# Performance work log

Measured on AMD Instinct MI355X. Metric: run time of the kernel, lower is better.

Reference implementation:

```python
import jax, jax.numpy as jnp
import numpy as np
from jax import lax

B, T_IN, T_OUT, E, U, V = 32, 128, 128, 512, 512, 9000


def reverse_seq(x, lens):
    # tf.reverse_sequence along time axis 1
    T = x.shape[1]
    t = jnp.arange(T)[None, :]
    idx = jnp.where(t < lens[:, None], lens[:, None] - 1 - t, t)
    return jnp.take_along_axis(x, idx[:, :, None], axis=1)


def run_lstm(x, lens, kernel, bias):
    """TF LSTMCell (gate order i,j,f,o, forget_bias=1.0) with dynamic_rnn
    length semantics: zero outputs and frozen state past seq_len."""
    T = x.shape[1]
    units = bias.shape[0] // 4
    xT = jnp.swapaxes(x, 0, 1)  # [T,B,D]
    c0 = jnp.zeros((x.shape[0], units), x.dtype)
    h0 = jnp.zeros_like(c0)

    def step(carry, xs):
        c, h = carry
        xt, t = xs
        z = jnp.concatenate([xt, h], axis=-1) @ kernel + bias
        i, j, f, o = jnp.split(z, 4, axis=-1)
        c_new = jax.nn.sigmoid(f + 1.0) * c + jax.nn.sigmoid(i) * jnp.tanh(j)
        h_new = jax.nn.sigmoid(o) * jnp.tanh(c_new)
        valid = (t < lens)[:, None]
        c2 = jnp.where(valid, c_new, c)
        h2 = jnp.where(valid, h_new, h)
        out = jnp.where(valid, h_new, 0.0)
        return (c2, h2), out

    (c, h), outs = lax.scan(step, (c0, h0), (xT, jnp.arange(T)))
    return jnp.swapaxes(outs, 0, 1), (c, h)


def setup_inputs() -> dict:
    key = jax.random.key(0)
    ks = jax.random.split(key, 20)
    s = 0.05
    inp = {
        "embed_in": jax.random.normal(ks[0], (B, T_IN, E), jnp.float32),
        "dec_embed": jax.random.normal(ks[1], (B, T_OUT, E), jnp.float32),
        "in_seq_len": jax.random.randint(ks[2], (B,), T_IN // 2, T_IN + 1).astype(jnp.int32),
        # encoder fw/bw LSTM (input E, units U)
        "enc_fw_kernel": jax.random.normal(ks[3], (E + U, 4 * U), jnp.float32) * s,
        "enc_fw_bias": jnp.zeros((4 * U,), jnp.float32),
        "enc_bw_kernel": jax.random.normal(ks[4], (E + U, 4 * U), jnp.float32) * s,
        "enc_bw_bias": jnp.zeros((4 * U,), jnp.float32),
        # decoder layer0 input = concat(embed, attention) -> E+U
        "dec_kernel0": jax.random.normal(ks[5], (E + U + U, 4 * U), jnp.float32) * s,
        "dec_bias0": jnp.zeros((4 * U,), jnp.float32),
        "dec_kernel1": jax.random.normal(ks[6], (U + U, 4 * U), jnp.float32) * s,
        "dec_bias1": jnp.zeros((4 * U,), jnp.float32),
        # normalized Bahdanau attention
        "w_mem": jax.random.normal(ks[7], (2 * U, U), jnp.float32) * s,
        "w_query": jax.random.normal(ks[8], (U, U), jnp.float32) * s,
        "b_attn": jnp.zeros((U,), jnp.float32),
        "v_attn": jax.random.normal(ks[9], (U,), jnp.float32),
        "g_attn": jnp.asarray(np.sqrt(1.0 / U), jnp.float32),
        # attention layer: Linear(concat(cell_out, context)) no bias
        "w_attn_layer": jax.random.normal(ks[10], (U + 2 * U, U), jnp.float32) * s,
        # output projection to vocab
        "w_proj": jax.random.normal(ks[11], (U, V), jnp.float32) * s,
        "b_proj": jnp.zeros((V,), jnp.float32),
    }
    return inp


def reference(embed_in, dec_embed, in_seq_len,
              enc_fw_kernel, enc_fw_bias, enc_bw_kernel, enc_bw_bias,
              dec_kernel0, dec_bias0, dec_kernel1, dec_bias1,
              w_mem, w_query, b_attn, v_attn, g_attn,
              w_attn_layer, w_proj, b_proj):
    lens = in_seq_len
    # ---- bidirectional encoder ----
    fw_out, (c_fw, h_fw) = run_lstm(embed_in, lens, enc_fw_kernel, enc_fw_bias)
    x_rev = reverse_seq(embed_in, lens)
    bw_out_rev, (c_bw, h_bw) = run_lstm(x_rev, lens, enc_bw_kernel, enc_bw_bias)
    bw_out = reverse_seq(bw_out_rev, lens)
    enc_out = jnp.concatenate([fw_out, bw_out], axis=-1)  # [B,Tin,2U]

    # ---- normalized Bahdanau attention precompute ----
    keys = jnp.einsum('btd,du->btu', enc_out, w_mem)  # [B,Tin,U]
    v_norm = g_attn * v_attn / jnp.sqrt(jnp.sum(v_attn * v_attn))
    t_idx = jnp.arange(enc_out.shape[1])[None, :]
    attn_mask = t_idx < lens[:, None]  # [B,Tin]
    neg = jnp.asarray(-1e9, enc_out.dtype)

    # decoder initial state from encoder final states (fw->layer0, bw->layer1)
    a0 = jnp.zeros((embed_in.shape[0], keys.shape[-1]), embed_in.dtype)
    carry0 = (c_fw, h_fw, c_bw, h_bw, a0)

    def lstm_step(xt, c, h, kernel, bias):
        z = jnp.concatenate([xt, h], axis=-1) @ kernel + bias
        i, j, f, o = jnp.split(z, 4, axis=-1)
        c_new = jax.nn.sigmoid(f + 1.0) * c + jax.nn.sigmoid(i) * jnp.tanh(j)
        h_new = jax.nn.sigmoid(o) * jnp.tanh(c_new)
        return c_new, h_new

    def dec_step(carry, x_t):
        c0, h0, c1, h1, attn = carry
        cell_in = jnp.concatenate([x_t, attn], axis=-1)  # AttentionWrapper input
        c0n, h0n = lstm_step(cell_in, c0, h0, dec_kernel0, dec_bias0)
        c1n, h1n = lstm_step(h0n, c1, h1, dec_kernel1, dec_bias1)
        q = h1n @ w_query  # [B,U]
        score = jnp.einsum('btu,u->bt', jnp.tanh(keys + q[:, None, :] + b_attn), v_norm)
        score = jnp.where(attn_mask, score, neg)
        alpha = jax.nn.softmax(score, axis=-1)
        context = jnp.einsum('bt,btd->bd', alpha, enc_out)  # [B,2U]
        attn_new = jnp.concatenate([h1n, context], axis=-1) @ w_attn_layer  # [B,U]
        return (c0n, h0n, c1n, h1n, attn_new), attn_new

    xT = jnp.swapaxes(dec_embed, 0, 1)  # [Tout,B,E]
    _, dec_outs = lax.scan(dec_step, carry0, xT)
    dec_outs = jnp.swapaxes(dec_outs, 0, 1)  # [B,Tout,U]
    logits = dec_outs @ w_proj + b_proj  # [B,Tout,V]
    return logits
```

## Files before the change

### kernel.cpp

```cpp
#include <hip/hip_runtime.h>
#include <stdint.h>

#define NTHR 256
#define NBLKS 512

namespace cfg {
constexpr size_t F_CELLS = 0;
constexpr size_t F_H0    = 32768;
constexpr size_t F_C0    = 49152;
constexpr size_t F_H1    = 65536;
constexpr size_t F_C1    = 81920;
constexpr size_t F_ATTNS = 114688;
constexpr size_t F_VN    = 147456;
constexpr size_t F_ESUM  = 147968;
constexpr size_t F_CTXR  = 148480;
constexpr size_t F_AALL  = 181248;
constexpr size_t F_EOUT  = 2278400;
constexpr size_t F_KEYS  = 6472704;
constexpr size_t F_TOTAL = 8569856;
constexpr size_t MEMSET_BYTES = F_VN * 4;
constexpr size_t O_P0 = 0;
constexpr size_t O_P1 = 786432;
}

__device__ __forceinline__ float sigm(float x)   { return 1.0f / (1.0f + __expf(-x)); }
__device__ __forceinline__ float tanhft(float x) { return 1.0f - 2.0f / (1.0f + __expf(2.0f * x)); }

__device__ __forceinline__ float cload(const float* p) {
  return __hip_atomic_load(p, __ATOMIC_RELAXED, __HIP_MEMORY_SCOPE_AGENT);
}
__device__ __forceinline__ void cstore(float* p, float v) {
  __hip_atomic_store(p, v, __ATOMIC_RELAXED, __HIP_MEMORY_SCOPE_AGENT);
}

__device__ __forceinline__ void gbar(unsigned ep, unsigned* arr, unsigned* rel) {
  __syncthreads();
  if (blockIdx.x == 0) {
    if (threadIdx.x == 0)
      __hip_atomic_store(arr, ep, __ATOMIC_RELAXED, __HIP_MEMORY_SCOPE_AGENT);
    int s0 = threadIdx.x, s1 = threadIdx.x + 256;
    while (__hip_atomic_load(arr + s0, __ATOMIC_RELAXED, __HIP_MEMORY_SCOPE_AGENT) < ep)
      __builtin_amdgcn_s_sleep(1);
    while (__hip_atomic_load(arr + s1, __ATOMIC_RELAXED, __HIP_MEMORY_SCOPE_AGENT) < ep)
      __builtin_amdgcn_s_sleep(1);
    __syncthreads();
    __hip_atomic_store(rel + (size_t)s0 * 32, ep, __ATOMIC_RELAXED, __HIP_MEMORY_SCOPE_AGENT);
    __hip_atomic_store(rel + (size_t)s1 * 32, ep, __ATOMIC_RELAXED, __HIP_MEMORY_SCOPE_AGENT);
    __syncthreads();
  } else {
    if (threadIdx.x == 0) {
      __hip_atomic_store(arr + blockIdx.x, ep, __ATOMIC_RELAXED, __HIP_MEMORY_SCOPE_AGENT);
      while (__hip_atomic_load(rel + (size_t)blockIdx.x * 32, __ATOMIC_RELAXED,
                               __HIP_MEMORY_SCOPE_AGENT) < ep)
        __builtin_amdgcn_s_sleep(1);
    }
    __syncthreads();
  }
}

template<int KWIN, typename F>
__device__ __forceinline__ void stage(float* at, F&& f) {
  static_assert((32 * KWIN) % NTHR == 0, "tile must tile NTHR");
  constexpr int PER = (32 * KWIN) / NTHR;
  __syncthreads();
  float v[PER];
#pragma unroll
  for (int r = 0; r < PER; r++) {
    int i = threadIdx.x + NTHR * r;
    v[r] = f(i / KWIN, i % KWIN);
  }
#pragma unroll
  for (int r = 0; r < PER; r++) at[threadIdx.x + NTHR * r] = v[r];
  __syncthreads();
}

template<int KWIN>
__device__ __forceinline__ void gemm_frag(const float* __restrict__ W, int ldw,
                                          int n, bool nok, int kw0,
                                          const float* at, float* acc) {
  const int wave = threadIdx.x >> 6;
  constexpr int KQ = KWIN / 4;
  const int klo = wave * KQ;
  const float* wp = W + (size_t)(kw0 + klo) * (size_t)ldw + n;
  float w[KQ];
#pragma unroll
  for (int j = 0; j < KQ; j++) w[j] = nok ? wp[(size_t)j * ldw] : 0.f;
#pragma unroll
  for (int jj = 0; jj < KQ; jj += 4) {
    const float* ap = at + klo + jj;
#pragma unroll
    for (int m = 0; m < 32; m++) {
      float4 a = *(const float4*)(ap + m * KWIN);
      acc[m] = fmaf(a.x, w[jj + 0], acc[m]);
      acc[m] = fmaf(a.y, w[jj + 1], acc[m]);
      acc[m] = fmaf(a.z, w[jj + 2], acc[m]);
      acc[m] = fmaf(a.w, w[jj + 3], acc[m]);
    }
  }
}

__device__ __forceinline__ void red_write(float* red, const float* acc) {
  const int wave = threadIdx.x >> 6, lane = threadIdx.x & 63;
  __syncthreads();
#pragma unroll
  for (int m = 0; m < 32; m++) red[(wave * 32 + m) * 64 + lane] = acc[m];
  __syncthreads();
}
__device__ __forceinline__ float redsum(const float* red, int m, int c) {
  return red[m * 64 + c] + red[2048 + m * 64 + c] +
         red[4096 + m * 64 + c] + red[6144 + m * 64 + c];
}

__device__ __forceinline__ void epi_cstore(const float* red, float* outp, int ldo, int n0) {
  for (int i = threadIdx.x; i < 2048; i += NTHR) {
    int m = i >> 6, nn = i & 63;
    cstore(outp + (size_t)m * ldo + n0 + nn, redsum(red, m, nn));
  }
}

template<int NKB>
__device__ __forceinline__ void gate_sum4(const float* base, float g4[4]) {
  float v[4][NKB];
#pragma unroll
  for (int g = 0; g < 4; g++) {
    const float* p = base + g * 512;
#pragma unroll
    for (int j = 0; j < NKB; j++) v[g][j] = cload(p + (size_t)j * 65536);
  }
#pragma unroll
  for (int g = 0; g < 4; g++) {
    float s = 0.f;
#pragma unroll
    for (int j = 0; j < NKB; j++) s += v[g][j];
    g4[g] = s;
  }
}

__global__ __launch_bounds__(NTHR, 2) void seq2seq_kernel(
    const float* __restrict__ embed_in, const float* __restrict__ dec_embed,
    const int* __restrict__ lens,
    const float* __restrict__ Wfw, const float* __restrict__ bfw,
    const float* __restrict__ Wbw, const float* __restrict__ bbw,
    const float* __restrict__ Wd0, const float* __restrict__ bd0,
    const float* __restrict__ Wd1, const float* __restrict__ bd1,
    const float* __restrict__ Wmem, const float* __restrict__ Wq,
    const float* __restrict__ battn, const float* __restrict__ vattn,
    const float* __restrict__ gattn, const float* __restrict__ Wal,
    const float* __restrict__ Wproj, const float* __restrict__ bproj,
    float* __restrict__ out, float* ws) {
  __shared__ float smem[12288];
  float* at  = smem;
  float* red = smem + 4096;

  unsigned* arr = (unsigned*)ws;
  unsigned* rel = (unsigned*)ws + 512;
  float* h0     = ws + cfg::F_H0;
  float* c0     = ws + cfg::F_C0;
  float* h1     = ws + cfg::F_H1;
  float* c1     = ws + cfg::F_C1;
  float* attn_s = ws + cfg::F_ATTNS;
  float* vn     = ws + cfg::F_VN;
  float* esum   = ws + cfg::F_ESUM;
  float* ctxr   = ws + cfg::F_CTXR;
  float* aall   = ws + cfg::F_AALL;
  float* eout   = ws + cfg::F_EOUT;
  float* keysp  = ws + cfg::F_KEYS;
  float* p0     = out + cfg::O_P0;
  float* p1     = out + cfg::O_P1;

  const int bid = blockIdx.x, tid = threadIdx.x;
  const int wave = tid >> 6, lane = tid & 63;
  unsigned ep = 1;
#define BAR()  do { gbar(ep, arr, rel); ep++; } while (0)
#define BARSEAL() do { __threadfence(); gbar(ep, arr, rel); ep++; __threadfence(); } while (0)

  if (bid == 0) {
    float s = 0.f;
    for (int u = tid; u < 512; u += NTHR) { float x = vattn[u]; s = fmaf(x, x, s); }
#pragma unroll
    for (int off = 32; off > 0; off >>= 1) s += __shfl_xor(s, off, 64);
    if (lane == 0) at[64 + wave] = s;
    __syncthreads();
    float S = at[64] + at[65] + at[66] + at[67];
    float scale = gattn[0] / sqrtf(S);
    for (int u = tid; u < 512; u += NTHR) vn[u] = vattn[u] * scale;
  }
  BAR();

  for (int t = 0; t < 128; t++) {
    {
      int dir = bid >> 8;
      int r = bid & 255;
      int nb = r & 31, kb = r >> 5;
      const float* W = dir ? Wbw : Wfw;
      const float* hs = dir ? h1 : h0;
      stage<128>(at, [&](int m, int kl) -> float {
        int kk = kb * 128 + kl;
        if (kk < 512) {
          int tt = t;
          if (dir) { int len = lens[m]; tt = (t < len) ? (len - 1 - t) : t; }
          return embed_in[((size_t)m * 128 + tt) * 512 + kk];
        }
        return cload(hs + m * 512 + kk - 512);
      });
      float acc[32];
#pragma unroll
      for (int m = 0; m < 32; m++) acc[m] = 0.f;
      gemm_frag<128>(W, 2048, nb * 64 + lane, true, kb * 128, at, acc);
      red_write(red, acc);
      epi_cstore(red, (dir ? p1 : p0) + (size_t)kb * 65536, 2048, nb * 64);
    }
    BAR();
    if (bid < 128) {
      int dir = bid >> 6;
      int p = (bid & 63) * NTHR + tid;
      int m = p >> 9, u = p & 511;
      const float* parts = dir ? p1 : p0;
      const float* bias  = dir ? bbw : bfw;
      float* hs = dir ? h1 : h0;
      float* cs = dir ? (c1 + 16384) : c0;
      float g4[4];
      gate_sum4<8>(parts + m * 2048 + u, g4);
#pragma unroll
      for (int g = 0; g < 4; g++) g4[g] += bias[g * 512 + u];
      int len = lens[m];
      bool valid = t < len;
      float co = cload(cs + m * 512 + u);
      float cn = sigm(g4[2] + 1.f) * co + sigm(g4[0]) * tanhft(g4[1]);
      float hn = sigm(g4[3]) * tanhft(cn);
      if (valid) { cstore(cs + m * 512 + u, cn); cstore(hs + m * 512 + u, hn); }
      int tpos = dir ? (valid ? (len - 1 - t) : t) : t;
      eout[((size_t)m * 128 + tpos) * 1024 + dir * 512 + u] = valid ? hn : 0.f;
    }
    BAR();
  }

  BARSEAL();

  {
#pragma unroll 1
    for (int task = bid; task < 1024; task += NBLKS) {
      int mt = task >> 3, nb = task & 7;
      int n0 = nb * 64;
      const float* arow = eout + (size_t)mt * 32 * 1024;
      float acc[32];
#pragma unroll
      for (int m = 0; m < 32; m++) acc[m] = 0.f;
      const int n = n0 + lane;
#pragma unroll 1
      for (int c = 0; c < 8; c++) {
        stage<128>(at, [&](int m, int kl) -> float {
          return arow[(size_t)m * 1024 + c * 128 + kl];
        });
        gemm_frag<128>(Wmem, 512, n, true, c * 128, at, acc);
      }
      red_write(red, acc);
      for (int i = tid; i < 2048; i += NTHR) {
        int m = i >> 6, nn = i & 63;
        keysp[(size_t)mt * 32 * 512 + (size_t)m * 512 + n0 + nn] = redsum(red, m, nn);
      }
    }
  }
  BARSEAL();

  for (int t = 0; t < 128; t++) {
    if (bid < 384) {
      int nb = bid & 31, kb = bid >> 5;
      const float* asrc = attn_s + (size_t)((t + 1) & 1) * 16384;
      stage<128>(at, [&](int m, int kl) -> float {
        int kk = kb * 128 + kl;
        if (kk < 512) return dec_embed[((size_t)m * 128 + t) * 512 + kk];
        if (kk < 1024) return cload(asrc + m * 512 + kk - 512);
        return cload(h0 + m * 512 + kk - 1024);
      });
      float acc[32];
#pragma unroll
      for (int m = 0; m < 32; m++) acc[m] = 0.f;
      gemm_frag<128>(Wd0, 2048, nb * 64 + lane, true, kb * 128, at, acc);
      red_write(red, acc);
      epi_cstore(red, p0 + (size_t)kb * 65536, 2048, nb * 64);
    } else if (bid < 392 && t >= 1) {
      const float* asrc = attn_s + (size_t)((t + 1) & 1) * 16384;
      float v[8];
      int j8 = ((bid - 384) * 256 + tid) * 8;
#pragma unroll
      for (int k = 0; k < 8; k++) v[k] = cload(asrc + j8 + k);
#pragma unroll
      for (int k = 0; k < 8; k++) aall[(size_t)(t - 1) * 16384 + j8 + k] = v[k];
    }
    BAR();

    if (bid < 64) {
      int p = bid * NTHR + tid;
      int m = p >> 9, u = p & 511;
      float g4[4];
      gate_sum4<12>(p0 + m * 2048 + u, g4);
#pragma unroll
      for (int g = 0; g < 4; g++) g4[g] += bd0[g * 512 + u];
      float co = cload(c0 + m * 512 + u);
      float cn = sigm(g4[2] + 1.f) * co + sigm(g4[0]) * tanhft(g4[1]);
      float hn = sigm(g4[3]) * tanhft(cn);
      cstore(c0 + m * 512 + u, cn);
      cstore(h0 + m * 512 + u, hn);
    } else if (bid < 72) {
      float* az = attn_s + (size_t)(t & 1) * 16384 + (size_t)(bid - 64) * 2048;
      for (int i = tid; i < 2048; i += NTHR) cstore(az + i, 0.f);
    } else if (bid < 80) {
      float* cz = ctxr + (size_t)(bid - 72) * 4096;
      for (int i = tid; i < 4096; i += NTHR) cstore(cz + i, 0.f);
      if (bid == 72 && tid < 32) cstore(esum + tid, 0.f);
    }
    BAR();

    {
      int nb = bid & 31, kb = bid >> 5;
      stage<64>(at, [&](int m, int kl) -> float {
        int kk = kb * 64 + kl;
        return (kk < 512) ? cload(h0 + m * 512 + kk) : cload(h1 + m * 512 + kk - 512);
      });
      float acc[32];
#pragma unroll
      for (int m = 0; m < 32; m++) acc[m] = 0.f;
      gemm_frag<64>(Wd1, 2048, nb * 64 + lane, true, kb * 64, at, acc);
      red_write(red, acc);
      epi_cstore(red, p1 + (size_t)kb * 65536, 2048, nb * 64);
    }
    BAR();

    if (bid < 256) {
      const int b = bid >> 3, sub = bid & 7;
      const int len = lens[b];
      float* sh_h1v = at;
      float* sh_qb  = at + 512;
      float* sh_vnv = at + 1024;
      float* sh_e   = at + 1536;
      float* redq   = at + 2048;
      const float* c1r = c1 + (size_t)((t + 1) & 1) * 16384;
      float* c1w = c1 + (size_t)(t & 1) * 16384;
#pragma unroll 1
      for (int u = tid; u < 512; u += NTHR) {
        float g4[4];
        gate_sum4<16>(p1 + b * 2048 + u, g4);
#pragma unroll
        for (int g = 0; g < 4; g++) g4[g] += bd1[g * 512 + u];
        float co = cload(c1r + b * 512 + u);
        float cn = sigm(g4[2] + 1.f) * co + sigm(g4[0]) * tanhft(g4[1]);
        float hn = sigm(g4[3]) * tanhft(cn);
        if (sub == 0) {
          cstore(c1w + b * 512 + u, cn);
          cstore(h1 + b * 512 + u, hn);
        }
        sh_h1v[u] = hn;
        sh_vnv[u] = vn[u];
      }
      __syncthreads();
      {
        float4 qa = make_float4(0.f, 0.f, 0.f, 0.f), qb4 = make_float4(0.f, 0.f, 0.f, 0.f);
        const int ua = lane * 4, ub = 256 + lane * 4;
        const float* wqp = Wq + (size_t)(wave * 128) * 512;
#pragma unroll 1
        for (int kk = 0; kk < 128; kk += 8) {
          float4 wa[8], wb[8];
#pragma unroll
          for (int j = 0; j < 8; j++) {
            wa[j] = *(const float4*)(wqp + (size_t)(kk + j) * 512 + ua);
            wb[j] = *(const float4*)(wqp + (size_t)(kk + j) * 512 + ub);
          }
#pragma unroll
          for (int j = 0; j < 8; j++) {
            float h = sh_h1v[wave * 128 + kk + j];
            qa.x = fmaf(h, wa[j].x, qa.x); qa.y = fmaf(h, wa[j].y, qa.y);
            qa.z = fmaf(h, wa[j].z, qa.z); qa.w = fmaf(h, wa[j].w, qa.w);
            qb4.x = fmaf(h, wb[j].x, qb4.x); qb4.y = fmaf(h, wb[j].y, qb4.y);
            qb4.z = fmaf(h, wb[j].z, qb4.z); qb4.w = fmaf(h, wb[j].w, qb4.w);
          }
        }
        *(float4*)(redq + wave * 512 + ua) = qa;
        *(float4*)(redq + wave * 512 + ub) = qb4;
      }
      __syncthreads();
      for (int u = tid; u < 512; u += NTHR)
        sh_qb[u] = redq[u] + redq[512 + u] + redq[1024 + u] + redq[1536 + u] + battn[u];
      __syncthreads();
      {
        float4 kv[4][2];
#pragma unroll
        for (int j = 0; j < 4; j++) {
          const float* kp = keysp + ((size_t)b * 128 + sub * 16 + wave * 4 + j) * 512;
          kv[j][0] = *(const float4*)(kp + lane * 4);
          kv[j][1] = *(const float4*)(kp + lane * 4 + 256);
        }
#pragma unroll
        for (int j = 0; j < 4; j++) {
          int tq = sub * 16 + wave * 4 + j;
          float s = 0.f;
#pragma unroll
          for (int hh = 0; hh < 2; hh++) {
            int u = lane * 4 + hh * 256;
            float4 k4 = kv[j][hh];
            s += sh_vnv[u + 0] * tanhft(k4.x + sh_qb[u + 0]);
            s += sh_vnv[u + 1] * tanhft(k4.y + sh_qb[u + 1]);
            s += sh_vnv[u + 2] * tanhft(k4.z + sh_qb[u + 2]);
            s += sh_vnv[u + 3] * tanhft(k4.w + sh_qb[u + 3]);
          }
#pragma unroll
          for (int off = 32; off > 0; off >>= 1) s += __shfl_xor(s, off, 64);
          if (lane == 0) sh_e[wave * 4 + j] = (tq < len) ? __expf(s) : 0.f;
        }
      }
      __syncthreads();
      if (tid == 0) {
        float es = 0.f;
#pragma unroll
        for (int i = 0; i < 16; i++) es += sh_e[i];
        atomicAdd(esum + b, es);
      }
      {
        int d = tid * 4;
        const float* ep2 = eout + ((size_t)b * 128 + sub * 16) * 1024 + d;
        float4 e4[16];
#pragma unroll
        for (int j = 0; j < 16; j++)
          e4[j] = *(const float4*)(ep2 + (size_t)j * 1024);
        float4 acc = make_float4(0.f, 0.f, 0.f, 0.f);
#pragma unroll
        for (int j = 0; j < 16; j++) {
          float a = sh_e[j];
          acc.x = fmaf(a, e4[j].x, acc.x); acc.y = fmaf(a, e4[j].y, acc.y);
          acc.z = fmaf(a, e4[j].z, acc.z); acc.w = fmaf(a, e4[j].w, acc.w);
        }
        float* cp = ctxr + (size_t)b * 1024 + d;
        atomicAdd(cp + 0, acc.x);
        atomicAdd(cp + 1, acc.y);
        atomicAdd(cp + 2, acc.z);
        atomicAdd(cp + 3, acc.w);
      }
    }
    BAR();

    if (bid < 128) {
      int nb = bid & 7, kb = bid >> 3;
      stage<96>(at, [&](int m, int kl) -> float {
        int kk = kb * 96 + kl;
        if (kk < 512) return cload(h1 + m * 512 + kk);
        float inv = 1.0f / cload(esum + m);
        return cload(ctxr + (size_t)m * 1024 + kk - 512) * inv;
      });
      float acc[32];
#pragma unroll
      for (int m = 0; m < 32; m++) acc[m] = 0.f;
      gemm_frag<96>(Wal, 512, nb * 64 + lane, true, kb * 96, at, acc);
      red_write(red, acc);
      float* adst = attn_s + (size_t)(t & 1) * 16384;
      for (int i = tid; i < 2048; i += NTHR) {
        int m = i >> 6, nn = i & 63;
        atomicAdd(adst + (size_t)m * 512 + nb * 64 + nn, redsum(red, m, nn));
      }
    }
    BAR();
  }

  if (bid >= 384 && bid < 392) {
    const float* asrc = attn_s + (size_t)1 * 16384;
    float v[8];
    int j8 = ((bid - 384) * 256 + tid) * 8;
#pragma unroll
    for (int k = 0; k < 8; k++) v[k] = cload(asrc + j8 + k);
#pragma unroll
    for (int k = 0; k < 8; k++) aall[(size_t)127 * 16384 + j8 + k] = v[k];
  }
  BARSEAL();

#pragma unroll 1
  for (int task = bid; task < 564; task += NBLKS) {
    int nb = task >> 2, tq = task & 3;
    int n0 = nb * 64;
    const int col = n0 + lane;
    const bool ok = col < 9000;
#pragma unroll 1
    for (int t = tq * 32; t < tq * 32 + 32; t++) {
      const float* asrc = aall + (size_t)t * 16384;
      float acc[32];
#pragma unroll
      for (int m = 0; m < 32; m++) acc[m] = 0.f;
#pragma unroll 1
      for (int c = 0; c < 4; c++) {
        stage<128>(at, [&](int m, int kl) -> float {
          return asrc[(size_t)m * 512 + c * 128 + kl];
        });
        gemm_frag<128>(Wproj, 9000, col, ok, c * 128, at, acc);
      }
      red_write(red, acc);
      for (int i = tid; i < 2048; i += NTHR) {
        int m = i >> 6, nn = i & 63;
        int nc = n0 + nn;
        if (nc < 9000)
          out[((size_t)m * 128 + t) * 9000 + nc] = redsum(red, m, nn) + bproj[nc];
      }
    }
  }
#undef BAR
#undef BARSEAL
}

extern "C" void kernel_launch(void* const* d_in, const int* in_sizes, int n_in,
                              void* d_out, int out_size, void* d_ws, size_t ws_size,
                              hipStream_t stream) {
  (void)in_sizes; (void)n_in; (void)out_size; (void)ws_size;
  hipMemsetAsync(d_ws, 0, cfg::MEMSET_BYTES, stream);
  hipLaunchKernelGGL(seq2seq_kernel, dim3(NBLKS), dim3(NTHR), 0, stream,
                     (const float*)d_in[0],
                     (const float*)d_in[1],
                     (const int*)d_in[2],
                     (const float*)d_in[3],
                     (const float*)d_in[4],
                     (const float*)d_in[5],
                     (const float*)d_in[6],
                     (const float*)d_in[7],
                     (const float*)d_in[8],
                     (const float*)d_in[9],
                     (const float*)d_in[10],
                     (const float*)d_in[11],
                     (const float*)d_in[12],
                     (const float*)d_in[13],
                     (const float*)d_in[14],
                     (const float*)d_in[15],
                     (const float*)d_in[16],
                     (const float*)d_in[17],
                     (const float*)d_in[18],
                     (float*)d_out, (float*)d_ws);
}
```

Baseline: 18.39 ms.

## Hoist input projections out of recurrences and fold attention layer into precomputed encoder products

Before each recurrence, one batched GEMM computes the input-gate contributions for encoder fw/bw and decoder layer 0 (x@W_x for all timesteps), so the per-step GEMMs only multiply the hidden state. The attention output layer is split algebraically: enc_out@W_al is precomputed once alongside the keys, and the per-step context projection becomes an alpha-weighted sum of those rows plus h1@W_al computed inside the attention blocks. This removes one grid barrier per decoder step and shrinks the per-step GEMM work. The cost is larger scratch buffers in the output area and extra upfront GEMM work. The layer-1 input and recurrent GEMMs are also split so the recurrent half overlaps with layer 0.

```diff
diff --git a/kernel.cpp b/kernel.cpp
--- a/kernel.cpp
+++ b/kernel.cpp
@@ -10,17 +10,21 @@
 constexpr size_t F_C0    = 49152;
 constexpr size_t F_H1    = 65536;
 constexpr size_t F_C1    = 81920;
-constexpr size_t F_ATTNS = 114688;
-constexpr size_t F_VN    = 147456;
-constexpr size_t F_ESUM  = 147968;
-constexpr size_t F_CTXR  = 148480;
-constexpr size_t F_AALL  = 181248;
-constexpr size_t F_EOUT  = 2278400;
-constexpr size_t F_KEYS  = 6472704;
-constexpr size_t F_TOTAL = 8569856;
+constexpr size_t F_H1W   = 114688;
+constexpr size_t F_EATTN = 147456;
+constexpr size_t F_ESUM  = 180224;
+constexpr size_t F_VN    = 181248;
+constexpr size_t F_AALL  = 181760;
+constexpr size_t F_EOUT  = 2278912;
+constexpr size_t F_KEYS  = 6473216;
+constexpr size_t F_TOTAL = 8570368;
 constexpr size_t MEMSET_BYTES = F_VN * 4;
-constexpr size_t O_P0 = 0;
-constexpr size_t O_P1 = 786432;
+constexpr size_t O_P0    = 0;
+constexpr size_t O_P1    = 524288;
+constexpr size_t O_XGFW  = 1048576;
+constexpr size_t O_XGBW  = 9437184;
+constexpr size_t O_XGD0  = 17825792;
+constexpr size_t O_EOWAL = 26214400;
 }
 
 __device__ __forceinline__ float sigm(float x)   { return 1.0f / (1.0f + __expf(-x)); }
@@ -117,6 +121,12 @@
     cstore(outp + (size_t)m * ldo + n0 + nn, redsum(red, m, nn));
   }
 }
+__device__ __forceinline__ void epi_plain(const float* red, float* outp, int ldo, int n0) {
+  for (int i = threadIdx.x; i < 2048; i += NTHR) {
+    int m = i >> 6, nn = i & 63;
+    outp[(size_t)m * ldo + n0 + nn] = redsum(red, m, nn);
+  }
+}
 
 template<int NKB>
 __device__ __forceinline__ void gate_sum4(const float* base, float g4[4]) {
@@ -158,21 +168,32 @@
   float* c0     = ws + cfg::F_C0;
   float* h1     = ws + cfg::F_H1;
   float* c1     = ws + cfg::F_C1;
-  float* attn_s = ws + cfg::F_ATTNS;
+  float* h1w    = ws + cfg::F_H1W;
+  float* eattn  = ws + cfg::F_EATTN;
+  float* esum   = ws + cfg::F_ESUM;
   float* vn     = ws + cfg::F_VN;
-  float* esum   = ws + cfg::F_ESUM;
-  float* ctxr   = ws + cfg::F_CTXR;
   float* aall   = ws + cfg::F_AALL;
   float* eout   = ws + cfg::F_EOUT;
   float* keysp  = ws + cfg::F_KEYS;
   float* p0     = out + cfg::O_P0;
   float* p1     = out + cfg::O_P1;
+  float* xgfw   = out + cfg::O_XGFW;
+  float* xgbw   = out + cfg::O_XGBW;
+  float* xgd0   = out + cfg::O_XGD0;
+  float* eoWal  = out + cfg::O_EOWAL;
 
   const int bid = blockIdx.x, tid = threadIdx.x;
   const int wave = tid >> 6, lane = tid & 63;
   unsigned ep = 1;
 #define BAR()  do { gbar(ep, arr, rel); ep++; } while (0)
 #define BARSEAL() do { __threadfence(); gbar(ep, arr, rel); ep++; __threadfence(); } while (0)
+
+  auto attn_of = [&](const float* h1w_p, const float* ea_p, const float* es_p,
+                     int m, int u) -> float {
+    float es = cload(es_p + m);
+    float inv = es > 0.f ? 1.f / es : 0.f;
+    return cload(h1w_p + m * 512 + u) + cload(ea_p + m * 512 + u) * inv;
+  };
 
   if (bid == 0) {
     float s = 0.f;
@@ -184,29 +205,46 @@
     float S = at[64] + at[65] + at[66] + at[67];
     float scale = gattn[0] / sqrtf(S);
     for (int u = tid; u < 512; u += NTHR) vn[u] = vattn[u] * scale;
-  }
-  BAR();
+    __syncthreads();
+  }
+
+#pragma unroll 1
+  for (int task = bid; task < 12288; task += NBLKS) {
+    int mat = task >> 12;
+    int r = task & 4095;
+    int tt = r >> 5, nb = r & 31;
+    const float* X = (mat == 2) ? dec_embed : embed_in;
+    const float* W = (mat == 0) ? Wfw : (mat == 1) ? Wbw : Wd0;
+    float* dst = ((mat == 0) ? xgfw : (mat == 1) ? xgbw : xgd0) + (size_t)tt * 65536;
+    float acc[32];
+#pragma unroll
+    for (int m = 0; m < 32; m++) acc[m] = 0.f;
+#pragma unroll 1
+    for (int c = 0; c < 4; c++) {
+      stage<128>(at, [&](int m, int kl) -> float {
+        return X[((size_t)m * 128 + tt) * 512 + c * 128 + kl];
+      });
+      gemm_frag<128>(W, 2048, nb * 64 + lane, true, c * 128, at, acc);
+    }
+    red_write(red, acc);
+    epi_plain(red, dst, 2048, nb * 64);
+  }
+  BARSEAL();
 
   for (int t = 0; t < 128; t++) {
-    {
-      int dir = bid >> 8;
-      int r = bid & 255;
+    if (bid < 256) {
+      int dir = bid >> 7;
+      int r = bid & 127;
       int nb = r & 31, kb = r >> 5;
       const float* W = dir ? Wbw : Wfw;
       const float* hs = dir ? h1 : h0;
       stage<128>(at, [&](int m, int kl) -> float {
-        int kk = kb * 128 + kl;
-        if (kk < 512) {
-          int tt = t;
-          if (dir) { int len = lens[m]; tt = (t < len) ? (len - 1 - t) : t; }
-          return embed_in[((size_t)m * 128 + tt) * 512 + kk];
-        }
-        return cload(hs + m * 512 + kk - 512);
+        return cload(hs + m * 512 + kb * 128 + kl);
       });
       float acc[32];
 #pragma unroll
       for (int m = 0; m < 32; m++) acc[m] = 0.f;
-      gemm_frag<128>(W, 2048, nb * 64 + lane, true, kb * 128, at, acc);
+      gemm_frag<128>(W, 2048, nb * 64 + lane, true, 512 + kb * 128, at, acc);
       red_write(red, acc);
       epi_cstore(red, (dir ? p1 : p0) + (size_t)kb * 65536, 2048, nb * 64);
     }
@@ -219,12 +257,14 @@
       const float* bias  = dir ? bbw : bfw;
       float* hs = dir ? h1 : h0;
       float* cs = dir ? (c1 + 16384) : c0;
-      float g4[4];
-      gate_sum4<8>(parts + m * 2048 + u, g4);
-#pragma unroll
-      for (int g = 0; g < 4; g++) g4[g] += bias[g * 512 + u];
       int len = lens[m];
       bool valid = t < len;
+      int tt = dir ? ((t < len) ? (len - 1 - t) : t) : t;
+      const float* xg = (dir ? xgbw : xgfw) + (size_t)tt * 65536 + m * 2048;
+      float g4[4];
+      gate_sum4<4>(parts + m * 2048 + u, g4);
+#pragma unroll
+      for (int g = 0; g < 4; g++) g4[g] += xg[g * 512 + u] + bias[g * 512 + u];
       float co = cload(cs + m * 512 + u);
       float cn = sigm(g4[2] + 1.f) * co + sigm(g4[0]) * tanhft(g4[1]);
       float hn = sigm(g4[3]) * tanhft(cn);
@@ -234,94 +274,115 @@
     }
     BAR();
   }
-
   BARSEAL();
 
-  {
-#pragma unroll 1
-    for (int task = bid; task < 1024; task += NBLKS) {
+#pragma unroll 1
+  for (int task = bid; task < 2048; task += NBLKS) {
+    if (task < 1024) {
       int mt = task >> 3, nb = task & 7;
-      int n0 = nb * 64;
       const float* arow = eout + (size_t)mt * 32 * 1024;
       float acc[32];
 #pragma unroll
       for (int m = 0; m < 32; m++) acc[m] = 0.f;
-      const int n = n0 + lane;
 #pragma unroll 1
       for (int c = 0; c < 8; c++) {
         stage<128>(at, [&](int m, int kl) -> float {
           return arow[(size_t)m * 1024 + c * 128 + kl];
         });
-        gemm_frag<128>(Wmem, 512, n, true, c * 128, at, acc);
-      }
-      red_write(red, acc);
-      for (int i = tid; i < 2048; i += NTHR) {
-        int m = i >> 6, nn = i & 63;
-        keysp[(size_t)mt * 32 * 512 + (size_t)m * 512 + n0 + nn] = redsum(red, m, nn);
-      }
+        gemm_frag<128>(Wmem, 512, nb * 64 + lane, true, c * 128, at, acc);
+      }
+      red_write(red, acc);
+      epi_plain(red, keysp + (size_t)mt * 32 * 512, 512, nb * 64);
+    } else {
+      int t2 = task - 1024;
+      int mt = t2 >> 3, nb = t2 & 7;
+      const float* arow = eout + (size_t)mt * 32 * 1024;
+      float acc[32];
+#pragma unroll
+      for (int m = 0; m < 32; m++) acc[m] = 0.f;
+#pragma unroll 1
+      for (int c = 0; c < 8; c++) {
+        stage<128>(at, [&](int m, int kl) -> float {
+          return arow[(size_t)m * 1024 + c * 128 + kl];
+        });
+        gemm_frag<128>(Wal, 512, nb * 64 + lane, true, 512 + c * 128, at, acc);
+      }
+      red_write(red, acc);
+      epi_plain(red, eoWal + (size_t)mt * 32 * 512, 512, nb * 64);
     }
   }
   BARSEAL();
 
   for (int t = 0; t < 128; t++) {
-    if (bid < 384) {
+    const float* h1w_p = h1w + (size_t)((t + 1) & 1) * 16384;
+    const float* ea_p  = eattn + (size_t)((t + 1) & 1) * 16384;
+    const float* es_p  = esum + (size_t)((t + 1) & 1) * 512;
+
+    if (bid < 256) {
       int nb = bid & 31, kb = bid >> 5;
-      const float* asrc = attn_s + (size_t)((t + 1) & 1) * 16384;
       stage<128>(at, [&](int m, int kl) -> float {
         int kk = kb * 128 + kl;
-        if (kk < 512) return dec_embed[((size_t)m * 128 + t) * 512 + kk];
-        if (kk < 1024) return cload(asrc + m * 512 + kk - 512);
-        return cload(h0 + m * 512 + kk - 1024);
+        if (kk < 512) return attn_of(h1w_p, ea_p, es_p, m, kk);
+        return cload(h0 + m * 512 + kk - 512);
       });
       float acc[32];
 #pragma unroll
       for (int m = 0; m < 32; m++) acc[m] = 0.f;
-      gemm_frag<128>(Wd0, 2048, nb * 64 + lane, true, kb * 128, at, acc);
+      gemm_frag<128>(Wd0, 2048, nb * 64 + lane, true, 512 + kb * 128, at, acc);
       red_write(red, acc);
       epi_cstore(red, p0 + (size_t)kb * 65536, 2048, nb * 64);
+    } else if (bid < 384) {
+      int idx = bid - 256;
+      int nb = idx & 31, kb = idx >> 5;
+      stage<128>(at, [&](int m, int kl) -> float {
+        return cload(h1 + m * 512 + kb * 128 + kl);
+      });
+      float acc[32];
+#pragma unroll
+      for (int m = 0; m < 32; m++) acc[m] = 0.f;
+      gemm_frag<128>(Wd1, 2048, nb * 64 + lane, true, 512 + kb * 128, at, acc);
+      red_write(red, acc);
+      epi_cstore(red, p1 + (size_t)(4 + kb) * 65536, 2048, nb * 64);
     } else if (bid < 392 && t >= 1) {
-      const float* asrc = attn_s + (size_t)((t + 1) & 1) * 16384;
+      int j = (bid - 384) * 256 + tid;
+      int m = j >> 6, u0 = (j & 63) * 8;
       float v[8];
-      int j8 = ((bid - 384) * 256 + tid) * 8;
-#pragma unroll
-      for (int k = 0; k < 8; k++) v[k] = cload(asrc + j8 + k);
-#pragma unroll
-      for (int k = 0; k < 8; k++) aall[(size_t)(t - 1) * 16384 + j8 + k] = v[k];
+#pragma unroll
+      for (int k = 0; k < 8; k++) v[k] = attn_of(h1w_p, ea_p, es_p, m, u0 + k);
+#pragma unroll
+      for (int k = 0; k < 8; k++) aall[(size_t)(t - 1) * 16384 + m * 512 + u0 + k] = v[k];
     }
     BAR();
 
     if (bid < 64) {
       int p = bid * NTHR + tid;
       int m = p >> 9, u = p & 511;
+      const float* xg = xgd0 + (size_t)t * 65536 + m * 2048;
       float g4[4];
-      gate_sum4<12>(p0 + m * 2048 + u, g4);
-#pragma unroll
-      for (int g = 0; g < 4; g++) g4[g] += bd0[g * 512 + u];
+      gate_sum4<8>(p0 + m * 2048 + u, g4);
+#pragma unroll
+      for (int g = 0; g < 4; g++) g4[g] += xg[g * 512 + u] + bd0[g * 512 + u];
       float co = cload(c0 + m * 512 + u);
       float cn = sigm(g4[2] + 1.f) * co + sigm(g4[0]) * tanhft(g4[1]);
       float hn = sigm(g4[3]) * tanhft(cn);
       cstore(c0 + m * 512 + u, cn);
       cstore(h0 + m * 512 + u, hn);
     } else if (bid < 72) {
-      float* az = attn_s + (size_t)(t & 1) * 16384 + (size_t)(bid - 64) * 2048;
+      float* az = eattn + (size_t)(t & 1) * 16384 + (size_t)(bid - 64) * 2048;
       for (int i = tid; i < 2048; i += NTHR) cstore(az + i, 0.f);
-    } else if (bid < 80) {
-      float* cz = ctxr + (size_t)(bid - 72) * 4096;
-      for (int i = tid; i < 4096; i += NTHR) cstore(cz + i, 0.f);
-      if (bid == 72 && tid < 32) cstore(esum + tid, 0.f);
+      if (bid == 64 && tid < 32) cstore(esum + (size_t)(t & 1) * 512 + tid, 0.f);
     }
     BAR();
 
-    {
+    if (bid < 128) {
       int nb = bid & 31, kb = bid >> 5;
-      stage<64>(at, [&](int m, int kl) -> float {
-        int kk = kb * 64 + kl;
-        return (kk < 512) ? cload(h0 + m * 512 + kk) : cload(h1 + m * 512 + kk - 512);
+      stage<128>(at, [&](int m, int kl) -> float {
+        return cload(h0 + m * 512 + kb * 128 + kl);
       });
       float acc[32];
 #pragma unroll
       for (int m = 0; m < 32; m++) acc[m] = 0.f;
-      gemm_frag<64>(Wd1, 2048, nb * 64 + lane, true, kb * 64, at, acc);
+      gemm_frag<128>(Wd1, 2048, nb * 64 + lane, true, kb * 128, at, acc);
       red_write(red, acc);
       epi_cstore(red, p1 + (size_t)kb * 65536, 2048, nb * 64);
     }
@@ -334,13 +395,17 @@
       float* sh_qb  = at + 512;
       float* sh_vnv = at + 1024;
       float* sh_e   = at + 1536;
+      float* sh_hw  = at + 1568;
       float* redq   = at + 2048;
       const float* c1r = c1 + (size_t)((t + 1) & 1) * 16384;
       float* c1w = c1 + (size_t)(t & 1) * 16384;
+      float* h1w_w = h1w + (size_t)(t & 1) * 16384;
+      float* ea_w  = eattn + (size_t)(t & 1) * 16384;
+      float* es_w  = esum + (size_t)(t & 1) * 512;
 #pragma unroll 1
       for (int u = tid; u < 512; u += NTHR) {
         float g4[4];
-        gate_sum4<16>(p1 + b * 2048 + u, g4);
+        gate_sum4<8>(p1 + b * 2048 + u, g4);
 #pragma unroll
         for (int g = 0; g < 4; g++) g4[g] += bd1[g * 512 + u];
         float co = cload(c1r + b * 512 + u);
@@ -413,61 +478,61 @@
         float es = 0.f;
 #pragma unroll
         for (int i = 0; i < 16; i++) es += sh_e[i];
-        atomicAdd(esum + b, es);
+        atomicAdd(es_w + b, es);
       }
       {
-        int d = tid * 4;
-        const float* ep2 = eout + ((size_t)b * 128 + sub * 16) * 1024 + d;
-        float4 e4[16];
-#pragma unroll
-        for (int j = 0; j < 16; j++)
-          e4[j] = *(const float4*)(ep2 + (size_t)j * 1024);
-        float4 acc = make_float4(0.f, 0.f, 0.f, 0.f);
+        int u2 = tid * 2;
+        const float* wp2 = eoWal + ((size_t)b * 128 + sub * 16) * 512 + u2;
+        float r0[16], r1[16];
 #pragma unroll
         for (int j = 0; j < 16; j++) {
-          float a = sh_e[j];
-          acc.x = fmaf(a, e4[j].x, acc.x); acc.y = fmaf(a, e4[j].y, acc.y);
-          acc.z = fmaf(a, e4[j].z, acc.z); acc.w = fmaf(a, e4[j].w, acc.w);
-        }
-        float* cp = ctxr + (size_t)b * 1024 + d;
-        atomicAdd(cp + 0, acc.x);
-        atomicAdd(cp + 1, acc.y);
-        atomicAdd(cp + 2, acc.z);
-        atomicAdd(cp + 3, acc.w);
+          r0[j] = wp2[(size_t)j * 512];
+          r1[j] = wp2[(size_t)j * 512 + 1];
+        }
+        float a0 = 0.f, a1 = 0.f;
+#pragma unroll
+        for (int j = 0; j < 16; j++) {
+          a0 = fmaf(sh_e[j], r0[j], a0);
+          a1 = fmaf(sh_e[j], r1[j], a1);
+        }
+        atomicAdd(ea_w + b * 512 + u2, a0);
+        atomicAdd(ea_w + b * 512 + u2 + 1, a1);
+      }
+      {
+        int col = tid & 63, kq = tid >> 6;
+        const float* wp2 = Wal + (size_t)(kq * 128) * 512 + sub * 64 + col;
+        float pacc = 0.f;
+#pragma unroll 1
+        for (int k0 = 0; k0 < 128; k0 += 32) {
+          float wv[32];
+#pragma unroll
+          for (int j = 0; j < 32; j++) wv[j] = wp2[(size_t)(k0 + j) * 512];
+#pragma unroll
+          for (int j = 0; j < 32; j++)
+            pacc = fmaf(sh_h1v[kq * 128 + k0 + j], wv[j], pacc);
+        }
+        sh_hw[tid] = pacc;
+        __syncthreads();
+        if (tid < 64) {
+          float s = sh_hw[tid] + sh_hw[64 + tid] + sh_hw[128 + tid] + sh_hw[192 + tid];
+          cstore(h1w_w + b * 512 + sub * 64 + tid, s);
+        }
       }
     }
     BAR();
-
-    if (bid < 128) {
-      int nb = bid & 7, kb = bid >> 3;
-      stage<96>(at, [&](int m, int kl) -> float {
-        int kk = kb * 96 + kl;
-        if (kk < 512) return cload(h1 + m * 512 + kk);
-        float inv = 1.0f / cload(esum + m);
-        return cload(ctxr + (size_t)m * 1024 + kk - 512) * inv;
-      });
-      float acc[32];
-#pragma unroll
-      for (int m = 0; m < 32; m++) acc[m] = 0.f;
-      gemm_frag<96>(Wal, 512, nb * 64 + lane, true, kb * 96, at, acc);
-      red_write(red, acc);
-      float* adst = attn_s + (size_t)(t & 1) * 16384;
-      for (int i = tid; i < 2048; i += NTHR) {
-        int m = i >> 6, nn = i & 63;
-        atomicAdd(adst + (size_t)m * 512 + nb * 64 + nn, redsum(red, m, nn));
-      }
-    }
-    BAR();
   }
 
   if (bid >= 384 && bid < 392) {
-    const float* asrc = attn_s + (size_t)1 * 16384;
+    const float* h1w_p = h1w + (size_t)1 * 16384;
+    const float* ea_p  = eattn + (size_t)1 * 16384;
+    const float* es_p  = esum + (size_t)1 * 512;
+    int j = (bid - 384) * 256 + tid;
+    int m = j >> 6, u0 = (j & 63) * 8;
     float v[8];
-    int j8 = ((bid - 384) * 256 + tid) * 8;
-#pragma unroll
-    for (int k = 0; k < 8; k++) v[k] = cload(asrc + j8 + k);
-#pragma unroll
-    for (int k = 0; k < 8; k++) aall[(size_t)127 * 16384 + j8 + k] = v[k];
+#pragma unroll
+    for (int k = 0; k < 8; k++) v[k] = attn_of(h1w_p, ea_p, es_p, m, u0 + k);
+#pragma unroll
+    for (int k = 0; k < 8; k++) aall[(size_t)127 * 16384 + m * 512 + u0 + k] = v[k];
   }
   BARSEAL();
 
```

Result: faster. 16.19 ms (-12.0%).
